# Kernel tuning notes

Measured on AMD Instinct MI355X. Metric: run time of the kernel, lower is better.

The kernel has to match this reference:

```python
import jax, jax.numpy as jnp
import numpy as np

PF_DIM = 1024
F_DIM = 1024
LOW = 128
MID = 32  # low_dim // 4
BATCH = 8192


def setup_inputs() -> dict:
    key = jax.random.key(0)
    ks = jax.random.split(key, 10)
    s = lambda fan_in: 1.0 / np.sqrt(fan_in)
    return {
        "f": jax.random.normal(ks[0], (BATCH, F_DIM), jnp.float32),
        "pf": jax.random.normal(ks[1], (BATCH, PF_DIM), jnp.float32),
        # nn.Linear weights are (out, in)
        "proj_f_w": jax.random.uniform(ks[2], (LOW, F_DIM), jnp.float32, -s(F_DIM), s(F_DIM)),
        "proj_f_b": jax.random.uniform(ks[3], (LOW,), jnp.float32, -s(F_DIM), s(F_DIM)),
        "proj_pf_w": jax.random.uniform(ks[4], (LOW, PF_DIM), jnp.float32, -s(PF_DIM), s(PF_DIM)),
        "proj_pf_b": jax.random.uniform(ks[5], (LOW,), jnp.float32, -s(PF_DIM), s(PF_DIM)),
        "proj_f2_w": jax.random.uniform(ks[6], (F_DIM, LOW), jnp.float32, -s(LOW), s(LOW)),
        "proj_f2_b": jax.random.uniform(ks[7], (F_DIM,), jnp.float32, -s(LOW), s(LOW)),
        "pg_w": jax.random.uniform(ks[8], (2 * LOW * MID, LOW), jnp.float32, -s(LOW), s(LOW)),
        "pg_b": jax.random.uniform(ks[9], (2 * LOW * MID,), jnp.float32, -s(LOW), s(LOW)),
    }


def reference(f, pf, proj_f_w, proj_f_b, proj_pf_w, proj_pf_b,
              proj_f2_w, proj_f2_b, pg_w, pg_b):
    b = pf.shape[0]
    # project both inputs to low_dim
    f_low = f @ proj_f_w.T + proj_f_b              # (b, LOW)
    pf_low = pf @ proj_pf_w.T + proj_pf_b          # (b, LOW)
    # per-sample generated weights
    params = pf_low @ pg_w.T + pg_b                # (b, 2*LOW*MID)
    dim = LOW * MID
    p1 = params[:, :dim].reshape(b, LOW, MID)      # (b, LOW, MID)
    p2 = params[:, dim:].reshape(b, MID, LOW)      # (b, MID, LOW)
    # batched tiny MLP: (b,1,LOW)@(b,LOW,MID) -> relu -> @(b,MID,LOW)
    h = jax.nn.relu(jnp.einsum('bl,blm->bm', f_low, p1))
    g = jnp.einsum('bm,bml->bl', h, p2)            # (b, LOW)
    out = g @ proj_f2_w.T + proj_f2_b + f + pf     # (b, F_DIM)
    return out
```

## Files before the change

### kernel.cpp

```cpp
#include <hip/hip_runtime.h>
#include <stdint.h>


typedef __attribute__((ext_vector_type(8))) short bf16x8;
typedef __attribute__((ext_vector_type(4))) float f32x4;

#define MFMA(a, b, c) __builtin_amdgcn_mfma_f32_16x16x32_bf16((a), (b), (c), 0, 0, 0)

__device__ __forceinline__ ushort f2bf(float x) {
    union { float f; uint32_t u; } v; v.f = x;
    return (ushort)((v.u + 0x7FFFu + ((v.u >> 16) & 1u)) >> 16);
}
__device__ __forceinline__ ushort4 f2bf4(float4 v) {
    ushort4 o; o.x = f2bf(v.x); o.y = f2bf(v.y); o.z = f2bf(v.z); o.w = f2bf(v.w); return o;
}
__device__ __forceinline__ float bf2f(ushort u) {
    union { uint32_t i; float f; } v; v.i = ((uint32_t)u) << 16; return v.f;
}

__global__ __launch_bounds__(256) void k0_convert(
    const float* __restrict__ pgw, const float* __restrict__ wf,
    const float* __restrict__ wpf, const float* __restrict__ w2,
    ushort* __restrict__ pg_img, ushort* __restrict__ w_img, ushort* __restrict__ w2_img)
{
    int cid = blockIdx.x * 256 + threadIdx.x;
    const float* src; ushort* dst;
    if (cid < 131072) {
        int lane = cid & 63, ks = (cid >> 6) & 3, T = cid >> 8;
        int j = T * 16 + (lane & 15), k = ks * 32 + (lane >> 4) * 8;
        src = pgw + (size_t)j * 128 + k;
        dst = pg_img + (size_t)cid * 8;
    } else if (cid < 163840) {
        int c = cid - 131072;
        int lane = c & 63, ks = (c >> 6) & 31, lt = (c >> 11) & 7, mat = c >> 14;
        int l = lt * 16 + (lane & 15), k = ks * 32 + (lane >> 4) * 8;
        src = (mat ? wpf : wf) + (size_t)l * 1024 + k;
        dst = w_img + (size_t)c * 8;
    } else {
        int c = cid - 163840;
        int lane = c & 63, ks = (c >> 6) & 3, nt = c >> 8;
        int n = nt * 16 + (lane & 15), k = ks * 32 + (lane >> 4) * 8;
        src = w2 + (size_t)n * 128 + k;
        dst = w2_img + (size_t)c * 8;
    }
    float4 a = ((const float4*)src)[0], b = ((const float4*)src)[1];
    ((ushort4*)dst)[0] = f2bf4(a);
    ((ushort4*)dst)[1] = f2bf4(b);
}

__global__ __launch_bounds__(512, 2) void mega(
    const float* __restrict__ f, const float* __restrict__ pf,
    const ushort* __restrict__ w_img, const float* __restrict__ bfb,
    const float* __restrict__ bpfb, const ushort* __restrict__ pg_img,
    const float* __restrict__ pgb, const ushort* __restrict__ w2_img,
    const float* __restrict__ b2, float* __restrict__ out)
{
    __shared__ __align__(16) char smem[62464];
    ushort* As    = (ushort*)smem;
    ushort* Tr    = (ushort*)smem;
    float*  hred  = (float*)smem;
    float*  hl    = (float*)(smem + 16896);
    float*  gLDS  = (float*)smem;
    float*  Ls    = (float*)smem;
    ushort* flowT = (ushort*)(smem + 36864);
    ushort* pfrag = (ushort*)(smem + 46080);
    ushort* gfrag = (ushort*)(smem + 54272);

    const int tid = threadIdx.x;
    const int lane = tid & 63, wid = tid >> 6;
    const int q = lane >> 4, r15 = lane & 15;
    const int b0 = blockIdx.x * 32;

    {
        float4 vbuf[8];
#pragma unroll
        for (int rr = 0; rr < 8; rr++) {
            int row = rr * 4 + (tid >> 7);
            vbuf[rr] = *(const float4*)(f + (size_t)(b0 + row) * 1024 + (tid & 127) * 4);
        }
        f32x4 c[2];
        float bias_v = 0.f;
#pragma unroll
        for (int s = 0; s < 4; s++) {
            const int mat = s >> 1, kh = s & 1;
            if (kh == 0) {
                c[0] = (f32x4){0.f, 0.f, 0.f, 0.f};
                c[1] = (f32x4){0.f, 0.f, 0.f, 0.f};
                bias_v = (mat ? bpfb : bfb)[wid * 16 + r15];
            }
            __syncthreads();
#pragma unroll
            for (int rr = 0; rr < 8; rr++) {
                int row = rr * 4 + (tid >> 7);
                *(ushort4*)(As + row * 520 + (tid & 127) * 4) = f2bf4(vbuf[rr]);
            }
            __syncthreads();
            if (s < 3) {
                const int sn = s + 1, matn = sn >> 1, khn = sn & 1;
                const float* srcn = matn ? pf : f;
#pragma unroll
                for (int rr = 0; rr < 8; rr++) {
                    int row = rr * 4 + (tid >> 7);
                    vbuf[rr] = *(const float4*)(srcn + (size_t)(b0 + row) * 1024 + khn * 512 + (tid & 127) * 4);
                }
            }
            const ushort* wb = w_img + (size_t)mat * 131072 + ((size_t)wid * 32 + kh * 16) * 512;
            bf16x8 wfr[4];
#pragma unroll
            for (int p = 0; p < 4; p++) wfr[p] = *(const bf16x8*)(wb + (size_t)p * 512 + lane * 8);
#pragma unroll
            for (int ks = 0; ks < 16; ks++) {
                const int cur = ks & 3;
                bf16x8 a0 = *(const bf16x8*)(As + (size_t)r15 * 520 + ks * 32 + q * 8);
                bf16x8 a1 = *(const bf16x8*)(As + (size_t)(16 + r15) * 520 + ks * 32 + q * 8);
                c[0] = MFMA(a0, wfr[cur], c[0]);
                c[1] = MFMA(a1, wfr[cur], c[1]);
                if (ks + 4 < 16)
                    wfr[cur] = *(const bf16x8*)(wb + (size_t)(ks + 4) * 512 + lane * 8);
            }
            if (s == 1) {
                int l = wid * 16 + r15;
#pragma unroll
                for (int mt = 0; mt < 2; mt++)
#pragma unroll
                    for (int r = 0; r < 4; r++)
                        flowT[l * 36 + mt * 16 + q * 4 + r] = f2bf(c[mt][r] + bias_v);
            }
            if (s == 3) {
                __syncthreads();
                int l = wid * 16 + r15;
#pragma unroll
                for (int mt = 0; mt < 2; mt++)
#pragma unroll
                    for (int r = 0; r < 4; r++)
                        Tr[(mt * 16 + q * 4 + r) * 136 + l] = f2bf(c[mt][r] + bias_v);
                __syncthreads();
                int bt = wid >> 2, ks2 = wid & 3;
                int k0 = ks2 * 32 + (lane >> 4) * 8;
                uint4 tv = *(const uint4*)(Tr + (size_t)(bt * 16 + (lane & 15)) * 136 + k0);
                *(uint4*)(pfrag + (size_t)wid * 512 + lane * 8) = tv;
            }
        }
    }
    __syncthreads();

    bf16x8 bfr[2][4];
#pragma unroll
    for (int ct = 0; ct < 2; ct++)
#pragma unroll
        for (int ks = 0; ks < 4; ks++)
            bfr[ct][ks] = *(const bf16x8*)(pfrag + (size_t)(ct * 4 + ks) * 512 + lane * 8);

    {
        const int mh = wid & 1, lq = wid >> 1;
        f32x4 hacc[2];
        hacc[0] = (f32x4){0.f, 0.f, 0.f, 0.f};
        hacc[1] = (f32x4){0.f, 0.f, 0.f, 0.f};

        bf16x8 af[4][4];
        f32x4 bvr[4];
#pragma unroll
        for (int t = 0; t < 4; t++) {
            const int T = (lq * 32 + t) * 2 + mh;
            const ushort* ap = pg_img + (size_t)T * 2048;
#pragma unroll
            for (int ks = 0; ks < 4; ks++)
                af[t][ks] = *(const bf16x8*)(ap + ks * 512 + lane * 8);
            bvr[t] = *(const f32x4*)(pgb + (size_t)T * 16 + q * 4);
        }
#pragma unroll 1
        for (int to = 0; to < 8; to++) {
#pragma unroll
            for (int ti = 0; ti < 4; ti++) {
                const int t = to * 4 + ti;
                const int l = lq * 32 + t;
                f32x4 bv = bvr[ti];
#pragma unroll
                for (int ct = 0; ct < 2; ct++) {
                    f32x4 cc = (f32x4){0.f, 0.f, 0.f, 0.f};
#pragma unroll
                    for (int ks = 0; ks < 4; ks++) cc = MFMA(af[ti][ks], bfr[ct][ks], cc);
                    float s = bf2f(flowT[l * 36 + ct * 16 + r15]);
#pragma unroll
                    for (int r = 0; r < 4; r++) hacc[ct][r] += s * (cc[r] + bv[r]);
                }
                if (t + 4 < 32) {
                    const int Tn = (l + 4) * 2 + mh;
                    const ushort* ap = pg_img + (size_t)Tn * 2048;
#pragma unroll
                    for (int ks = 0; ks < 4; ks++)
                        af[ti][ks] = *(const bf16x8*)(ap + ks * 512 + lane * 8);
                    bvr[ti] = *(const f32x4*)(pgb + (size_t)Tn * 16 + q * 4);
                }
            }
        }
#pragma unroll
        for (int ct = 0; ct < 2; ct++)
#pragma unroll
            for (int r = 0; r < 4; r++)
                hred[lq * 1056 + (mh * 16 + q * 4 + r) * 33 + ct * 16 + r15] = hacc[ct][r];
    }
    __syncthreads();
    {
        int m = tid >> 4, bc = (tid & 15) * 2;
        float s0 = 0.f, s1 = 0.f;
#pragma unroll
        for (int w = 0; w < 4; w++) {
            s0 += hred[w * 1056 + m * 33 + bc];
            s1 += hred[w * 1056 + m * 33 + bc + 1];
        }
        hl[m * 32 + bc]     = fmaxf(s0, 0.f);
        hl[m * 32 + bc + 1] = fmaxf(s1, 0.f);
    }
    __syncthreads();

    {
        f32x4 gacc[2];
        gacc[0] = (f32x4){0.f, 0.f, 0.f, 0.f};
        gacc[1] = (f32x4){0.f, 0.f, 0.f, 0.f};

        bf16x8 afc[4][4];
        f32x4 bvc[4];
#pragma unroll
        for (int t = 0; t < 4; t++) {
            const ushort* ap = pg_img + (size_t)(256 + t * 8 + wid) * 2048;
#pragma unroll
            for (int ks = 0; ks < 4; ks++)
                afc[t][ks] = *(const bf16x8*)(ap + ks * 512 + lane * 8);
            bvc[t] = *(const f32x4*)(pgb + 4096 + (size_t)t * 128 + wid * 16 + q * 4);
        }
#pragma unroll 1
        for (int mo = 0; mo < 8; mo++) {
#pragma unroll
            for (int mi = 0; mi < 4; mi++) {
                const int m = mo * 4 + mi;
                f32x4 bv = bvc[mi];
#pragma unroll
                for (int ct = 0; ct < 2; ct++) {
                    f32x4 cc = (f32x4){0.f, 0.f, 0.f, 0.f};
#pragma unroll
                    for (int ks = 0; ks < 4; ks++) cc = MFMA(afc[mi][ks], bfr[ct][ks], cc);
                    float s = hl[m * 32 + ct * 16 + r15];
#pragma unroll
                    for (int r = 0; r < 4; r++) gacc[ct][r] += s * (cc[r] + bv[r]);
                }
                if (m + 4 < 32) {
                    const int mn = m + 4;
                    const ushort* ap = pg_img + (size_t)(256 + mn * 8 + wid) * 2048;
#pragma unroll
                    for (int ks = 0; ks < 4; ks++)
                        afc[mi][ks] = *(const bf16x8*)(ap + ks * 512 + lane * 8);
                    bvc[mi] = *(const f32x4*)(pgb + 4096 + (size_t)mn * 128 + wid * 16 + q * 4);
                }
            }
        }
#pragma unroll
        for (int ct = 0; ct < 2; ct++)
#pragma unroll
            for (int r = 0; r < 4; r++)
                gLDS[(size_t)(wid * 16 + q * 4 + r) * 33 + ct * 16 + r15] = gacc[ct][r];
    }
    __syncthreads();
    {
        const int bt = wid >> 2, ksl = wid & 3;
        const int bloc = bt * 16 + (lane & 15);
        const int l0 = ksl * 32 + (lane >> 4) * 8;
        ushort tmp[8];
#pragma unroll
        for (int e = 0; e < 8; e++)
            tmp[e] = f2bf(gLDS[(size_t)(l0 + e) * 33 + bloc]);
        ushort4 lo = {tmp[0], tmp[1], tmp[2], tmp[3]};
        ushort4 hi = {tmp[4], tmp[5], tmp[6], tmp[7]};
        ushort* dst = gfrag + (size_t)wid * 512 + lane * 8;
        ((ushort4*)dst)[0] = lo;
        ((ushort4*)dst)[1] = hi;
    }
    __syncthreads();

    {
        bf16x8 afg[2][4];
#pragma unroll
        for (int mtl = 0; mtl < 2; mtl++)
#pragma unroll
            for (int ks = 0; ks < 4; ks++)
                afg[mtl][ks] = *(const bf16x8*)(gfrag + (size_t)(mtl * 4 + ks) * 512 + lane * 8);

#pragma unroll 1
        for (int nb = 0; nb < 4; nb++) {
            const int n0 = nb * 256;
            float4 fa[4], pa[4];
#pragma unroll
            for (int rr = 0; rr < 4; rr++) {
                const int b = b0 + wid * 4 + rr;
                const size_t gbase = (size_t)b * 1024 + n0 + lane * 4;
                fa[rr] = *(const float4*)(f + gbase);
                pa[rr] = *(const float4*)(pf + gbase);
            }
            float bias_v2[2];
#pragma unroll
            for (int nt = 0; nt < 2; nt++) bias_v2[nt] = b2[nb * 256 + wid * 32 + nt * 16 + r15];
            bf16x8 w2r[2][4];
#pragma unroll
            for (int nt = 0; nt < 2; nt++)
#pragma unroll
                for (int ks = 0; ks < 4; ks++)
                    w2r[nt][ks] = *(const bf16x8*)(w2_img + (size_t)((nb * 16 + wid * 2 + nt) * 4 + ks) * 512 + lane * 8);
#pragma unroll
            for (int nt = 0; nt < 2; nt++) {
#pragma unroll
                for (int mtl = 0; mtl < 2; mtl++) {
                    f32x4 cc = (f32x4){0.f, 0.f, 0.f, 0.f};
#pragma unroll
                    for (int ks = 0; ks < 4; ks++) cc = MFMA(afg[mtl][ks], w2r[nt][ks], cc);
                    const int nloc = wid * 32 + nt * 16 + r15;
                    const int chunk = nloc >> 5, within = nloc & 31;
#pragma unroll
                    for (int r = 0; r < 4; r++)
                        Ls[(size_t)(mtl * 16 + q * 4 + r) * 288 + chunk * 36 + within] = cc[r] + bias_v2[nt];
                }
            }
            __syncthreads();
            {
                const float* ls = Ls + (size_t)(wid * 4) * 288 + (lane >> 3) * 36 + (lane & 7) * 4;
#pragma unroll
                for (int rr = 0; rr < 4; rr++) {
                    const int b = b0 + wid * 4 + rr;
                    const size_t gbase = (size_t)b * 1024 + n0 + lane * 4;
                    float4 lv = *(const float4*)(ls + rr * 288);
                    float4 o;
                    o.x = lv.x + fa[rr].x + pa[rr].x; o.y = lv.y + fa[rr].y + pa[rr].y;
                    o.z = lv.z + fa[rr].z + pa[rr].z; o.w = lv.w + fa[rr].w + pa[rr].w;
                    *(float4*)(out + gbase) = o;
                }
            }
            __syncthreads();
        }
    }
}

extern "C" void kernel_launch(void* const* d_in, const int* in_sizes, int n_in,
                              void* d_out, int out_size, void* d_ws, size_t ws_size,
                              hipStream_t stream)
{
    const float* f    = (const float*)d_in[0];
    const float* pf   = (const float*)d_in[1];
    const float* wf   = (const float*)d_in[2];
    const float* bfb  = (const float*)d_in[3];
    const float* wpf  = (const float*)d_in[4];
    const float* bpfb = (const float*)d_in[5];
    const float* w2   = (const float*)d_in[6];
    const float* b2   = (const float*)d_in[7];
    const float* pgw  = (const float*)d_in[8];
    const float* pgb  = (const float*)d_in[9];

    char* ws = (char*)d_ws;
    ushort* pg_img = (ushort*)(ws + 0);
    ushort* w_img  = (ushort*)(ws + 2097152);
    ushort* w2_img = (ushort*)(ws + 2621440);
    float*  out    = (float*)d_out;

    k0_convert<<<dim3(704), dim3(256), 0, stream>>>(pgw, wf, wpf, w2, pg_img, w_img, w2_img);
    mega<<<dim3(256), dim3(512), 0, stream>>>(f, pf, w_img, bfb, bpfb,
                                              pg_img, pgb, w2_img, b2, out);
}
```

Baseline: 164.9 us.

## Halve per-block batch tile to 16 rows and double grid size

Each block of the fused kernel now handles 16 batch rows instead of 32. The grid doubles to 512 blocks, shared memory is roughly halved, and launch bounds ask for 4 blocks per CU. The aim is to fill all CUs on the MI355X, since 256 blocks is about one block per CU, and to hide latency better. The cost is that every block re-streams the per-sample generator weights (pg_img) and the projection weights, so weight traffic per batch row doubles and each wave does fewer MFMAs per weight fragment it loads.

```diff
diff --git a/kernel.cpp b/kernel.cpp
--- a/kernel.cpp
+++ b/kernel.cpp
@@ -48,49 +48,48 @@
     ((ushort4*)dst)[1] = f2bf4(b);
 }
 
-__global__ __launch_bounds__(512, 2) void mega(
+__global__ __launch_bounds__(512, 4) void mega(
     const float* __restrict__ f, const float* __restrict__ pf,
     const ushort* __restrict__ w_img, const float* __restrict__ bfb,
     const float* __restrict__ bpfb, const ushort* __restrict__ pg_img,
     const float* __restrict__ pgb, const ushort* __restrict__ w2_img,
     const float* __restrict__ b2, float* __restrict__ out)
 {
-    __shared__ __align__(16) char smem[62464];
+    __shared__ __align__(16) char smem[31744];
     ushort* As    = (ushort*)smem;
     ushort* Tr    = (ushort*)smem;
     float*  hred  = (float*)smem;
-    float*  hl    = (float*)(smem + 16896);
+    float*  hl    = (float*)(smem + 8704);
     float*  gLDS  = (float*)smem;
     float*  Ls    = (float*)smem;
-    ushort* flowT = (ushort*)(smem + 36864);
-    ushort* pfrag = (ushort*)(smem + 46080);
-    ushort* gfrag = (ushort*)(smem + 54272);
+    ushort* flowT = (ushort*)(smem + 18432);
+    ushort* pfrag = (ushort*)(smem + 23552);
+    ushort* gfrag = (ushort*)(smem + 27648);
 
     const int tid = threadIdx.x;
     const int lane = tid & 63, wid = tid >> 6;
     const int q = lane >> 4, r15 = lane & 15;
-    const int b0 = blockIdx.x * 32;
-
-    {
-        float4 vbuf[8];
-#pragma unroll
-        for (int rr = 0; rr < 8; rr++) {
+    const int b0 = blockIdx.x * 16;
+
+    {
+        float4 vbuf[4];
+#pragma unroll
+        for (int rr = 0; rr < 4; rr++) {
             int row = rr * 4 + (tid >> 7);
             vbuf[rr] = *(const float4*)(f + (size_t)(b0 + row) * 1024 + (tid & 127) * 4);
         }
-        f32x4 c[2];
+        f32x4 c;
         float bias_v = 0.f;
 #pragma unroll
         for (int s = 0; s < 4; s++) {
             const int mat = s >> 1, kh = s & 1;
             if (kh == 0) {
-                c[0] = (f32x4){0.f, 0.f, 0.f, 0.f};
-                c[1] = (f32x4){0.f, 0.f, 0.f, 0.f};
+                c = (f32x4){0.f, 0.f, 0.f, 0.f};
                 bias_v = (mat ? bpfb : bfb)[wid * 16 + r15];
             }
             __syncthreads();
 #pragma unroll
-            for (int rr = 0; rr < 8; rr++) {
+            for (int rr = 0; rr < 4; rr++) {
                 int row = rr * 4 + (tid >> 7);
                 *(ushort4*)(As + row * 520 + (tid & 127) * 4) = f2bf4(vbuf[rr]);
             }
@@ -99,7 +98,7 @@
                 const int sn = s + 1, matn = sn >> 1, khn = sn & 1;
                 const float* srcn = matn ? pf : f;
 #pragma unroll
-                for (int rr = 0; rr < 8; rr++) {
+                for (int rr = 0; rr < 4; rr++) {
                     int row = rr * 4 + (tid >> 7);
                     vbuf[rr] = *(const float4*)(srcn + (size_t)(b0 + row) * 1024 + khn * 512 + (tid & 127) * 4);
                 }
@@ -112,50 +111,41 @@
             for (int ks = 0; ks < 16; ks++) {
                 const int cur = ks & 3;
                 bf16x8 a0 = *(const bf16x8*)(As + (size_t)r15 * 520 + ks * 32 + q * 8);
-                bf16x8 a1 = *(const bf16x8*)(As + (size_t)(16 + r15) * 520 + ks * 32 + q * 8);
-                c[0] = MFMA(a0, wfr[cur], c[0]);
-                c[1] = MFMA(a1, wfr[cur], c[1]);
+                c = MFMA(a0, wfr[cur], c);
                 if (ks + 4 < 16)
                     wfr[cur] = *(const bf16x8*)(wb + (size_t)(ks + 4) * 512 + lane * 8);
             }
             if (s == 1) {
                 int l = wid * 16 + r15;
 #pragma unroll
-                for (int mt = 0; mt < 2; mt++)
-#pragma unroll
-                    for (int r = 0; r < 4; r++)
-                        flowT[l * 36 + mt * 16 + q * 4 + r] = f2bf(c[mt][r] + bias_v);
+                for (int r = 0; r < 4; r++)
+                    flowT[l * 20 + q * 4 + r] = f2bf(c[r] + bias_v);
             }
             if (s == 3) {
                 __syncthreads();
                 int l = wid * 16 + r15;
 #pragma unroll
-                for (int mt = 0; mt < 2; mt++)
-#pragma unroll
-                    for (int r = 0; r < 4; r++)
-                        Tr[(mt * 16 + q * 4 + r) * 136 + l] = f2bf(c[mt][r] + bias_v);
+                for (int r = 0; r < 4; r++)
+                    Tr[(q * 4 + r) * 136 + l] = f2bf(c[r] + bias_v);
                 __syncthreads();
-                int bt = wid >> 2, ks2 = wid & 3;
-                int k0 = ks2 * 32 + (lane >> 4) * 8;
-                uint4 tv = *(const uint4*)(Tr + (size_t)(bt * 16 + (lane & 15)) * 136 + k0);
-                *(uint4*)(pfrag + (size_t)wid * 512 + lane * 8) = tv;
-            }
-        }
-    }
-    __syncthreads();
-
-    bf16x8 bfr[2][4];
-#pragma unroll
-    for (int ct = 0; ct < 2; ct++)
-#pragma unroll
-        for (int ks = 0; ks < 4; ks++)
-            bfr[ct][ks] = *(const bf16x8*)(pfrag + (size_t)(ct * 4 + ks) * 512 + lane * 8);
+                if (wid < 4) {
+                    int k0 = wid * 32 + (lane >> 4) * 8;
+                    uint4 tv = *(const uint4*)(Tr + (size_t)(lane & 15) * 136 + k0);
+                    *(uint4*)(pfrag + (size_t)wid * 512 + lane * 8) = tv;
+                }
+            }
+        }
+    }
+    __syncthreads();
+
+    bf16x8 bfr[4];
+#pragma unroll
+    for (int ks = 0; ks < 4; ks++)
+        bfr[ks] = *(const bf16x8*)(pfrag + (size_t)ks * 512 + lane * 8);
 
     {
         const int mh = wid & 1, lq = wid >> 1;
-        f32x4 hacc[2];
-        hacc[0] = (f32x4){0.f, 0.f, 0.f, 0.f};
-        hacc[1] = (f32x4){0.f, 0.f, 0.f, 0.f};
+        f32x4 hacc = (f32x4){0.f, 0.f, 0.f, 0.f};
 
         bf16x8 af[4][4];
         f32x4 bvr[4];
@@ -175,15 +165,12 @@
                 const int t = to * 4 + ti;
                 const int l = lq * 32 + t;
                 f32x4 bv = bvr[ti];
-#pragma unroll
-                for (int ct = 0; ct < 2; ct++) {
-                    f32x4 cc = (f32x4){0.f, 0.f, 0.f, 0.f};
-#pragma unroll
-                    for (int ks = 0; ks < 4; ks++) cc = MFMA(af[ti][ks], bfr[ct][ks], cc);
-                    float s = bf2f(flowT[l * 36 + ct * 16 + r15]);
-#pragma unroll
-                    for (int r = 0; r < 4; r++) hacc[ct][r] += s * (cc[r] + bv[r]);
-                }
+                f32x4 cc = (f32x4){0.f, 0.f, 0.f, 0.f};
+#pragma unroll
+                for (int ks = 0; ks < 4; ks++) cc = MFMA(af[ti][ks], bfr[ks], cc);
+                float s = bf2f(flowT[l * 20 + r15]);
+#pragma unroll
+                for (int r = 0; r < 4; r++) hacc[r] += s * (cc[r] + bv[r]);
                 if (t + 4 < 32) {
                     const int Tn = (l + 4) * 2 + mh;
                     const ushort* ap = pg_img + (size_t)Tn * 2048;
@@ -195,29 +182,21 @@
             }
         }
 #pragma unroll
-        for (int ct = 0; ct < 2; ct++)
-#pragma unroll
-            for (int r = 0; r < 4; r++)
-                hred[lq * 1056 + (mh * 16 + q * 4 + r) * 33 + ct * 16 + r15] = hacc[ct][r];
-    }
-    __syncthreads();
-    {
-        int m = tid >> 4, bc = (tid & 15) * 2;
-        float s0 = 0.f, s1 = 0.f;
-#pragma unroll
-        for (int w = 0; w < 4; w++) {
-            s0 += hred[w * 1056 + m * 33 + bc];
-            s1 += hred[w * 1056 + m * 33 + bc + 1];
-        }
-        hl[m * 32 + bc]     = fmaxf(s0, 0.f);
-        hl[m * 32 + bc + 1] = fmaxf(s1, 0.f);
-    }
-    __syncthreads();
-
-    {
-        f32x4 gacc[2];
-        gacc[0] = (f32x4){0.f, 0.f, 0.f, 0.f};
-        gacc[1] = (f32x4){0.f, 0.f, 0.f, 0.f};
+        for (int r = 0; r < 4; r++)
+            hred[lq * 544 + (mh * 16 + q * 4 + r) * 17 + r15] = hacc[r];
+    }
+    __syncthreads();
+    {
+        int m = tid >> 4, bc = tid & 15;
+        float s = 0.f;
+#pragma unroll
+        for (int w = 0; w < 4; w++) s += hred[w * 544 + m * 17 + bc];
+        hl[m * 16 + bc] = fmaxf(s, 0.f);
+    }
+    __syncthreads();
+
+    {
+        f32x4 gacc = (f32x4){0.f, 0.f, 0.f, 0.f};
 
         bf16x8 afc[4][4];
         f32x4 bvc[4];
@@ -235,15 +214,12 @@
             for (int mi = 0; mi < 4; mi++) {
                 const int m = mo * 4 + mi;
                 f32x4 bv = bvc[mi];
-#pragma unroll
-                for (int ct = 0; ct < 2; ct++) {
-                    f32x4 cc = (f32x4){0.f, 0.f, 0.f, 0.f};
-#pragma unroll
-                    for (int ks = 0; ks < 4; ks++) cc = MFMA(afc[mi][ks], bfr[ct][ks], cc);
-                    float s = hl[m * 32 + ct * 16 + r15];
-#pragma unroll
-                    for (int r = 0; r < 4; r++) gacc[ct][r] += s * (cc[r] + bv[r]);
-                }
+                f32x4 cc = (f32x4){0.f, 0.f, 0.f, 0.f};
+#pragma unroll
+                for (int ks = 0; ks < 4; ks++) cc = MFMA(afc[mi][ks], bfr[ks], cc);
+                float s = hl[m * 16 + r15];
+#pragma unroll
+                for (int r = 0; r < 4; r++) gacc[r] += s * (cc[r] + bv[r]);
                 if (m + 4 < 32) {
                     const int mn = m + 4;
                     const ushort* ap = pg_img + (size_t)(256 + mn * 8 + wid) * 2048;
@@ -255,20 +231,17 @@
             }
         }
 #pragma unroll
-        for (int ct = 0; ct < 2; ct++)
-#pragma unroll
-            for (int r = 0; r < 4; r++)
-                gLDS[(size_t)(wid * 16 + q * 4 + r) * 33 + ct * 16 + r15] = gacc[ct][r];
-    }
-    __syncthreads();
-    {
-        const int bt = wid >> 2, ksl = wid & 3;
-        const int bloc = bt * 16 + (lane & 15);
-        const int l0 = ksl * 32 + (lane >> 4) * 8;
+        for (int r = 0; r < 4; r++)
+            gLDS[(size_t)(wid * 16 + q * 4 + r) * 17 + r15] = gacc[r];
+    }
+    __syncthreads();
+    if (wid < 4) {
+        const int bloc = lane & 15;
+        const int l0 = wid * 32 + (lane >> 4) * 8;
         ushort tmp[8];
 #pragma unroll
         for (int e = 0; e < 8; e++)
-            tmp[e] = f2bf(gLDS[(size_t)(l0 + e) * 33 + bloc]);
+            tmp[e] = f2bf(gLDS[(size_t)(l0 + e) * 17 + bloc]);
         ushort4 lo = {tmp[0], tmp[1], tmp[2], tmp[3]};
         ushort4 hi = {tmp[4], tmp[5], tmp[6], tmp[7]};
         ushort* dst = gfrag + (size_t)wid * 512 + lane * 8;
@@ -278,20 +251,18 @@
     __syncthreads();
 
     {
-        bf16x8 afg[2][4];
-#pragma unroll
-        for (int mtl = 0; mtl < 2; mtl++)
-#pragma unroll
-            for (int ks = 0; ks < 4; ks++)
-                afg[mtl][ks] = *(const bf16x8*)(gfrag + (size_t)(mtl * 4 + ks) * 512 + lane * 8);
+        bf16x8 afg[4];
+#pragma unroll
+        for (int ks = 0; ks < 4; ks++)
+            afg[ks] = *(const bf16x8*)(gfrag + (size_t)ks * 512 + lane * 8);
 
 #pragma unroll 1
         for (int nb = 0; nb < 4; nb++) {
             const int n0 = nb * 256;
-            float4 fa[4], pa[4];
-#pragma unroll
-            for (int rr = 0; rr < 4; rr++) {
-                const int b = b0 + wid * 4 + rr;
+            float4 fa[2], pa[2];
+#pragma unroll
+            for (int rr = 0; rr < 2; rr++) {
+                const int b = b0 + wid * 2 + rr;
                 const size_t gbase = (size_t)b * 1024 + n0 + lane * 4;
                 fa[rr] = *(const float4*)(f + gbase);
                 pa[rr] = *(const float4*)(pf + gbase);
@@ -307,24 +278,21 @@
                     w2r[nt][ks] = *(const bf16x8*)(w2_img + (size_t)((nb * 16 + wid * 2 + nt) * 4 + ks) * 512 + lane * 8);
 #pragma unroll
             for (int nt = 0; nt < 2; nt++) {
-#pragma unroll
-                for (int mtl = 0; mtl < 2; mtl++) {
-                    f32x4 cc = (f32x4){0.f, 0.f, 0.f, 0.f};
-#pragma unroll
-                    for (int ks = 0; ks < 4; ks++) cc = MFMA(afg[mtl][ks], w2r[nt][ks], cc);
-                    const int nloc = wid * 32 + nt * 16 + r15;
-                    const int chunk = nloc >> 5, within = nloc & 31;
-#pragma unroll
-                    for (int r = 0; r < 4; r++)
-                        Ls[(size_t)(mtl * 16 + q * 4 + r) * 288 + chunk * 36 + within] = cc[r] + bias_v2[nt];
-                }
+                f32x4 cc = (f32x4){0.f, 0.f, 0.f, 0.f};
+#pragma unroll
+                for (int ks = 0; ks < 4; ks++) cc = MFMA(afg[ks], w2r[nt][ks], cc);
+                const int nloc = wid * 32 + nt * 16 + r15;
+                const int chunk = nloc >> 5, within = nloc & 31;
+#pragma unroll
+                for (int r = 0; r < 4; r++)
+                    Ls[(size_t)(q * 4 + r) * 288 + chunk * 36 + within] = cc[r] + bias_v2[nt];
             }
             __syncthreads();
             {
-                const float* ls = Ls + (size_t)(wid * 4) * 288 + (lane >> 3) * 36 + (lane & 7) * 4;
-#pragma unroll
-                for (int rr = 0; rr < 4; rr++) {
-                    const int b = b0 + wid * 4 + rr;
+                const float* ls = Ls + (size_t)(wid * 2) * 288 + (lane >> 3) * 36 + (lane & 7) * 4;
+#pragma unroll
+                for (int rr = 0; rr < 2; rr++) {
+                    const int b = b0 + wid * 2 + rr;
                     const size_t gbase = (size_t)b * 1024 + n0 + lane * 4;
                     float4 lv = *(const float4*)(ls + rr * 288);
                     float4 o;
@@ -360,6 +328,6 @@
     float*  out    = (float*)d_out;
 
     k0_convert<<<dim3(704), dim3(256), 0, stream>>>(pgw, wf, wpf, w2, pg_img, w_img, w2_img);
-    mega<<<dim3(256), dim3(512), 0, stream>>>(f, pf, w_img, bfb, bpfb,
+    mega<<<dim3(512), dim3(512), 0, stream>>>(f, pf, w_img, bfb, bpfb,
                                               pg_img, pgb, w2_img, b2, out);
 }
```

New measurement: 274.8 us. 66.6% more time.

## Split fused mega kernel into two kernels passing h and pf_low via workspace

Applied to the files above, without the earlier changes.

Splits the single fused kernel into mega_ab (projections plus first generated-MLP layer) and mega_cd (second layer, output projection and residual). The intermediate relu(h) and the pf_low bf16 fragments go through global workspace buffers instead of staying in LDS. This may lower per-kernel register and LDS pressure or make each stage easier to profile. It costs an extra launch, a global round trip and a second pass over per-block state.

```diff
diff --git a/kernel.cpp b/kernel.cpp
--- a/kernel.cpp
+++ b/kernel.cpp
@@ -48,23 +48,19 @@
     ((ushort4*)dst)[1] = f2bf4(b);
 }
 
-__global__ __launch_bounds__(512, 2) void mega(
+__global__ __launch_bounds__(512, 2) void mega_ab(
     const float* __restrict__ f, const float* __restrict__ pf,
     const ushort* __restrict__ w_img, const float* __restrict__ bfb,
     const float* __restrict__ bpfb, const ushort* __restrict__ pg_img,
-    const float* __restrict__ pgb, const ushort* __restrict__ w2_img,
-    const float* __restrict__ b2, float* __restrict__ out)
+    const float* __restrict__ pgb,
+    float* __restrict__ h_g , ushort* __restrict__ pf_g )
 {
     __shared__ __align__(16) char smem[62464];
     ushort* As    = (ushort*)smem;
     ushort* Tr    = (ushort*)smem;
     float*  hred  = (float*)smem;
-    float*  hl    = (float*)(smem + 16896);
-    float*  gLDS  = (float*)smem;
-    float*  Ls    = (float*)smem;
     ushort* flowT = (ushort*)(smem + 36864);
     ushort* pfrag = (ushort*)(smem + 46080);
-    ushort* gfrag = (ushort*)(smem + 54272);
 
     const int tid = threadIdx.x;
     const int lane = tid & 63, wid = tid >> 6;
@@ -139,6 +135,7 @@
                 int k0 = ks2 * 32 + (lane >> 4) * 8;
                 uint4 tv = *(const uint4*)(Tr + (size_t)(bt * 16 + (lane & 15)) * 136 + k0);
                 *(uint4*)(pfrag + (size_t)wid * 512 + lane * 8) = tv;
+                *(uint4*)(pf_g + (size_t)blockIdx.x * 4096 + (size_t)wid * 512 + lane * 8) = tv;
             }
         }
     }
@@ -209,9 +206,41 @@
             s0 += hred[w * 1056 + m * 33 + bc];
             s1 += hred[w * 1056 + m * 33 + bc + 1];
         }
-        hl[m * 32 + bc]     = fmaxf(s0, 0.f);
-        hl[m * 32 + bc + 1] = fmaxf(s1, 0.f);
-    }
+        float2 hv;
+        hv.x = fmaxf(s0, 0.f);
+        hv.y = fmaxf(s1, 0.f);
+        *(float2*)(h_g + (size_t)blockIdx.x * 1024 + m * 32 + bc) = hv;
+    }
+}
+
+__global__ __launch_bounds__(512, 2) void mega_cd(
+    const float* __restrict__ f, const float* __restrict__ pf,
+    const ushort* __restrict__ pg_img, const float* __restrict__ pgb,
+    const ushort* __restrict__ w2_img, const float* __restrict__ b2,
+    const float* __restrict__ h_g, const ushort* __restrict__ pf_g,
+    float* __restrict__ out)
+{
+    __shared__ __align__(16) char smem[62464];
+    float*  hl    = (float*)smem;
+    float*  gLDS  = (float*)(smem + 4096);
+    float*  Ls    = (float*)smem;
+    ushort* gfrag = (ushort*)(smem + 54272);
+
+    const int tid = threadIdx.x;
+    const int lane = tid & 63, wid = tid >> 6;
+    const int q = lane >> 4, r15 = lane & 15;
+    const int b0 = blockIdx.x * 32;
+
+    {
+        float2 hv = *(const float2*)(h_g + (size_t)blockIdx.x * 1024 + tid * 2);
+        *(float2*)(hl + tid * 2) = hv;
+    }
+    bf16x8 bfr[2][4];
+#pragma unroll
+    for (int ct = 0; ct < 2; ct++)
+#pragma unroll
+        for (int ks = 0; ks < 4; ks++)
+            bfr[ct][ks] = *(const bf16x8*)(pf_g + (size_t)blockIdx.x * 4096 + (size_t)(ct * 4 + ks) * 512 + lane * 8);
     __syncthreads();
 
     {
@@ -357,9 +386,13 @@
     ushort* pg_img = (ushort*)(ws + 0);
     ushort* w_img  = (ushort*)(ws + 2097152);
     ushort* w2_img = (ushort*)(ws + 2621440);
+    float*  h_g    = (float*)(ws + 2883584);
+    ushort* pf_g   = (ushort*)(ws + 3932160);
     float*  out    = (float*)d_out;
 
     k0_convert<<<dim3(704), dim3(256), 0, stream>>>(pgw, wf, wpf, w2, pg_img, w_img, w2_img);
-    mega<<<dim3(256), dim3(512), 0, stream>>>(f, pf, w_img, bfb, bpfb,
-                                              pg_img, pgb, w2_img, b2, out);
-}
+    mega_ab<<<dim3(256), dim3(512), 0, stream>>>(f, pf, w_img, bfb, bpfb,
+                                                 pg_img, pgb, h_g, pf_g);
+    mega_cd<<<dim3(256), dim3(512), 0, stream>>>(f, pf, pg_img, pgb, w2_img, b2,
+                                                 h_g, pf_g, out);
+}
```

Result: slower. 172.9 us (+4.9%).
